# Kernel tuning notes

Hardware: AMD Instinct MI355X
Metric: run time of the kernel (lower is better)

Reference implementation:

```python
import jax, jax.numpy as jnp
import numpy as np

B_IMG, B_CAP, T_CAP, D = 64, 64, 64, 1024
H = D // 8          # CBN MLP bottleneck (k=8)
T_IMG = 36          # fixed number of image regions; cap_embed truncated to this
EPS = 1e-5          # BatchNorm eps
GAMMA = 10.0        # softmax gate temperature (norm_output=True)


def _l2norm(x, axis=-1):
    return x / jnp.linalg.norm(x, axis=axis, keepdims=True)


def setup_inputs() -> dict:
    key = jax.random.key(0)
    ks = jax.random.split(key, 8)
    s1 = 1.0 / np.sqrt(D)
    s2 = 1.0 / np.sqrt(H)
    return {
        "img_embed": jax.random.normal(ks[0], (B_IMG, T_IMG, D), jnp.float32),
        "cap_embed": jax.random.normal(ks[1], (B_CAP, T_CAP, D), jnp.float32),
        "lens": jax.random.randint(ks[2], (B_CAP,), 1, T_CAP + 1).astype(jnp.int32),
        # CondBatchNorm1d gamma/beta predictor MLPs: Linear(D,H)->ReLU->Linear(H,D)
        "Wg1": jax.random.normal(ks[3], (D, H), jnp.float32) * s1,
        "bg1": jnp.zeros((H,), jnp.float32),
        "Wg2": jax.random.normal(ks[4], (H, D), jnp.float32) * s2,
        "bg2": jnp.zeros((D,), jnp.float32),
        "Wb1": jax.random.normal(ks[5], (D, H), jnp.float32) * s1,
        "bb1": jnp.zeros((H,), jnp.float32),
        "Wb2": jax.random.normal(ks[6], (H, D), jnp.float32) * s2,
        "bb2": jnp.zeros((D,), jnp.float32),
    }


def reference(img_embed, cap_embed, lens, Wg1, bg1, Wg2, bg2, Wb1, bb1, Wb2, bb2):
    # permute to channels-first and truncate captions to 36 timesteps
    cap = jnp.transpose(cap_embed, (0, 2, 1))[:, :, :T_IMG]   # (Bc, D, 36)
    img = jnp.transpose(img_embed, (0, 2, 1))                 # (Bi, D, 36)
    img_repr = img.mean(-1)                                   # (Bi, D)

    # BatchNorm1d (affine=False), training-mode batch stats over (Bc, T) per channel.
    # cap is identical across the original per-image loop, so normalize once.
    mu = cap.mean(axis=(0, 2), keepdims=True)
    var = cap.var(axis=(0, 2), keepdims=True)
    xn = (cap - mu) / jnp.sqrt(var + EPS)                     # (Bc, D, 36)

    # condition-dependent gamma/beta per image (CBN: 1 + delta_gamma)
    gam = 1.0 + (jax.nn.relu(img_repr @ Wg1 + bg1) @ Wg2 + bg2)   # (Bi, D)
    bet = jax.nn.relu(img_repr @ Wb1 + bb1) @ Wb2 + bb2           # (Bi, D)

    # vectorized over the original Python loop: (Bi, Bc, D, 36)
    txt = gam[:, None, :, None] * xn[None] + bet[:, None, :, None]
    mask = jax.nn.softmax(txt * GAMMA, axis=-1)               # gate over time axis
    txt_vec = (mask * txt).mean(-1)                           # (Bi, Bc, D)

    txt_vec = _l2norm(txt_vec, -1)
    img_vec = _l2norm(img_repr, -1)                           # (Bi, D)
    sims = jnp.einsum("id,ibd->ib", img_vec, txt_vec)        # (Bi, Bc)
    return sims
```

## Files before the change

kernel.cpp:

```cpp
#include <hip/hip_runtime.h>
#include <hip/hip_bf16.h>

#define BI 64
#define BC 64
#define TCAP 64
#define D 1024
#define H 128
#define TIMG 36

__global__ __launch_bounds__(256) void k_pre(const float* __restrict__ img,
                                             const float* __restrict__ cap,
                                             const float* __restrict__ Wg1,
                                             const float* __restrict__ Wb1,
                                             float* __restrict__ repr,
                                             float* __restrict__ ivec,
                                             float* __restrict__ part,
                                             float* __restrict__ W1T) {
    int blk = blockIdx.x, tid = threadIdx.x;
    if (blk < 64) {
        int i = blk;
        const float4* base = (const float4*)(img + (size_t)i * TIMG * D);
        float4 s = {0.f, 0.f, 0.f, 0.f};
        for (int t = 0; t < TIMG; ++t) {
            float4 v = base[t * 256 + tid];
            s.x += v.x; s.y += v.y; s.z += v.z; s.w += v.w;
        }
        s.x *= (1.f / 36.f); s.y *= (1.f / 36.f); s.z *= (1.f / 36.f); s.w *= (1.f / 36.f);
        ((float4*)(repr + (size_t)i * D))[tid] = s;
        float local = s.x * s.x + s.y * s.y + s.z * s.z + s.w * s.w;
        for (int off = 32; off; off >>= 1) local += __shfl_xor(local, off);
        __shared__ float red[4];
        int wave = tid >> 6;
        if ((tid & 63) == 0) red[wave] = local;
        __syncthreads();
        float inv = rsqrtf(red[0] + red[1] + red[2] + red[3]);
        float4 o = {s.x * inv, s.y * inv, s.z * inv, s.w * inv};
        ((float4*)(ivec + (size_t)i * D))[tid] = o;
    } else if (blk < 128) {
        int b = blk - 64;
        const float4* base = (const float4*)(cap + (size_t)b * TCAP * D);
        float4 s = {0.f, 0.f, 0.f, 0.f}, ss = {0.f, 0.f, 0.f, 0.f};
        for (int t = 0; t < TIMG; ++t) {
            float4 v = base[t * 256 + tid];
            s.x += v.x; s.y += v.y; s.z += v.z; s.w += v.w;
            ss.x = fmaf(v.x, v.x, ss.x); ss.y = fmaf(v.y, v.y, ss.y);
            ss.z = fmaf(v.z, v.z, ss.z); ss.w = fmaf(v.w, v.w, ss.w);
        }
        ((float4*)(part + b * 2048))[tid] = s;
        ((float4*)(part + b * 2048 + 1024))[tid] = ss;
    } else {
        __shared__ float tile[64][65];
        int idx = blk - 128;
        int bx = idx & 15, by = (idx >> 4) & 1, bz = idx >> 5;
        const float* W = bz ? Wb1 : Wg1;
        int d0 = bx * 64, c0 = by * 64;
        int lane = tid & 63, w = tid >> 6;
#pragma unroll
        for (int k = 0; k < 16; ++k) {
            int dl = k * 4 + w;
            tile[dl][lane] = W[(size_t)(d0 + dl) * H + c0 + lane];
        }
        __syncthreads();
#pragma unroll
        for (int k = 0; k < 16; ++k) {
            int cl = k * 4 + w;
            W1T[(size_t)(bz * 128 + c0 + cl) * D + d0 + lane] = tile[lane][cl];
        }
    }
}

__global__ __launch_bounds__(256) void k_mid(const float* __restrict__ part,
                                             const float* __restrict__ repr,
                                             const float* __restrict__ W1T,
                                             const float* __restrict__ bg1,
                                             const float* __restrict__ bb1,
                                             float* __restrict__ mu,
                                             float* __restrict__ istd,
                                             float* __restrict__ hid) {
    int blk = blockIdx.x, tid = threadIdx.x;
    if (blk < 4) {
        int d = blk * 256 + tid;
        float s = 0.f, ss = 0.f;
        for (int g = 0; g < BC; ++g) {
            s += part[g * 2048 + d];
            ss += part[g * 2048 + 1024 + d];
        }
        const float invN = 1.f / 2304.f;
        float m = s * invN;
        float v = ss * invN - m * m;
        mu[d] = m;
        istd[d] = rsqrtf(v + 1e-5f);
    } else {
        int o = (blk - 4) * 4 + (tid >> 6);
        int lane = tid & 63;
        int i = o >> 8, c = o & 255;
        const float4* r = (const float4*)(repr + (size_t)i * D);
        const float4* w = (const float4*)(W1T + (size_t)c * D);
        float acc = 0.f;
#pragma unroll
        for (int k = 0; k < 4; ++k) {
            float4 rv = r[k * 64 + lane];
            float4 wv = w[k * 64 + lane];
            acc = fmaf(rv.x, wv.x, acc);
            acc = fmaf(rv.y, wv.y, acc);
            acc = fmaf(rv.z, wv.z, acc);
            acc = fmaf(rv.w, wv.w, acc);
        }
        for (int off = 32; off; off >>= 1) acc += __shfl_xor(acc, off);
        if (lane == 0) {
            float b = (c < 128) ? bg1[c] : bb1[c - 128];
            hid[o] = fmaxf(acc + b, 0.f);
        }
    }
}

__global__ __launch_bounds__(128) void k_out(const float* __restrict__ hid,
                                             const float* __restrict__ Wg2, const float* __restrict__ bg2,
                                             const float* __restrict__ Wb2, const float* __restrict__ bb2,
                                             float* __restrict__ gam, float* __restrict__ bet) {
    int i = blockIdx.x >> 2;
    int d2 = (blockIdx.x & 3) * 128 + threadIdx.x;
    __shared__ float h[256];
    h[threadIdx.x] = hid[i * 256 + threadIdx.x];
    h[128 + threadIdx.x] = hid[i * 256 + 128 + threadIdx.x];
    __syncthreads();
    float2 g = ((const float2*)bg2)[d2];
    float2 bb = ((const float2*)bb2)[d2];
#pragma unroll 4
    for (int hh = 0; hh < H; ++hh) {
        float2 wg = ((const float2*)(Wg2 + (size_t)hh * D))[d2];
        float2 wb = ((const float2*)(Wb2 + (size_t)hh * D))[d2];
        float hg = h[hh], hb = h[128 + hh];
        g.x = fmaf(hg, wg.x, g.x);
        g.y = fmaf(hg, wg.y, g.y);
        bb.x = fmaf(hb, wb.x, bb.x);
        bb.y = fmaf(hb, wb.y, bb.y);
    }
    float2 go = {1.f + g.x, 1.f + g.y};
    ((float2*)(gam + (size_t)i * D))[d2] = go;
    ((float2*)(bet + (size_t)i * D))[d2] = bb;
}

__global__ __launch_bounds__(512, 1) void k_main(const float* __restrict__ cap,
                                                 const float* __restrict__ mu,
                                                 const float* __restrict__ istd,
                                                 const float* __restrict__ gam,
                                                 const float* __restrict__ bet,
                                                 const float* __restrict__ ivec,
                                                 float* __restrict__ out) {
    int b = blockIdx.x, ig = blockIdx.y, tid = threadIdx.x;
    const float2* base = (const float2*)(cap + (size_t)b * TCAP * D);
    float2 mu2 = ((const float2*)mu)[tid];
    float2 is2 = ((const float2*)istd)[tid];
    const float A = 14.4269504089f;
    const float INV = 0.0693147180560f;

    float a0[16], a1[16], c0[16], c1[16];
    float sw0[16], sw1[16], sxa0[16], sxa1[16];
#pragma unroll
    for (int k = 0; k < 16; ++k) {
        int i = ig * 16 + k;
        float2 g = ((const float2*)(gam + (size_t)i * D))[tid];
        float2 be = ((const float2*)(bet + (size_t)i * D))[tid];
        a0[k] = A * g.x;
        a1[k] = A * g.y;
        c0[k] = A * (be.x - 6.f);
        c1[k] = A * (be.y - 6.f);
        sw0[k] = 0.f; sw1[k] = 0.f; sxa0[k] = 0.f; sxa1[k] = 0.f;
    }
#pragma unroll 2
    for (int t = 0; t < TIMG; ++t) {
        float2 cp = base[t * 512 + tid];
        float x0 = (cp.x - mu2.x) * is2.x;
        float x1 = (cp.y - mu2.y) * is2.y;
#pragma unroll
        for (int k = 0; k < 16; ++k) {
            float arg0 = fmaf(a0[k], x0, c0[k]);
            float e0 = __builtin_amdgcn_exp2f(arg0);
            sw0[k] += e0;
            sxa0[k] = fmaf(e0, arg0, sxa0[k]);
            float arg1 = fmaf(a1[k], x1, c1[k]);
            float e1 = __builtin_amdgcn_exp2f(arg1);
            sw1[k] += e1;
            sxa1[k] = fmaf(e1, arg1, sxa1[k]);
        }
    }
    __shared__ float redS[16][8], redD[16][8];
    int wave = tid >> 6;
#pragma unroll
    for (int k = 0; k < 16; ++k) {
        int i = ig * 16 + k;
        float2 iv = ((const float2*)(ivec + (size_t)i * D))[tid];
        float tv0 = fmaf(INV, sxa0[k] / sw0[k], 6.f);
        float tv1 = fmaf(INV, sxa1[k] / sw1[k], 6.f);
        float ss = tv0 * tv0 + tv1 * tv1;
        float sd = iv.x * tv0 + iv.y * tv1;
        for (int off = 32; off; off >>= 1) {
            ss += __shfl_xor(ss, off);
            sd += __shfl_xor(sd, off);
        }
        if ((tid & 63) == 0) { redS[k][wave] = ss; redD[k][wave] = sd; }
    }
    __syncthreads();
    if (tid < 128) {
        int k = tid >> 3, w = tid & 7;
        float s = redS[k][w], d = redD[k][w];
#pragma unroll
        for (int off = 1; off < 8; off <<= 1) {
            s += __shfl_xor(s, off);
            d += __shfl_xor(d, off);
        }
        if (w == 0) {
            int i = ig * 16 + k;
            out[i * BC + b] = d * rsqrtf(s);
        }
    }
}

extern "C" void kernel_launch(void* const* d_in, const int* in_sizes, int n_in,
                              void* d_out, int out_size, void* d_ws, size_t ws_size,
                              hipStream_t stream) {
    const float* img = (const float*)d_in[0];
    const float* cap = (const float*)d_in[1];
    const float* Wg1 = (const float*)d_in[3];
    const float* bg1 = (const float*)d_in[4];
    const float* Wg2 = (const float*)d_in[5];
    const float* bg2 = (const float*)d_in[6];
    const float* Wb1 = (const float*)d_in[7];
    const float* bb1 = (const float*)d_in[8];
    const float* Wb2 = (const float*)d_in[9];
    const float* bb2 = (const float*)d_in[10];

    float* ws = (float*)d_ws;
    float* repr = ws;
    float* ivec = ws + 65536;
    float* gam  = ws + 131072;
    float* bet  = ws + 196608;
    float* mu   = ws + 262144;
    float* istd = ws + 263168;
    float* part = ws + 264192;
    float* W1T  = ws + 395264;
    float* hid  = ws + 657408;
    float* out = (float*)d_out;

    k_pre<<<dim3(192), dim3(256), 0, stream>>>(img, cap, Wg1, Wb1, repr, ivec, part, W1T);
    k_mid<<<dim3(4100), dim3(256), 0, stream>>>(part, repr, W1T, bg1, bb1, mu, istd, hid);
    k_out<<<dim3(256), dim3(128), 0, stream>>>(hid, Wg2, bg2, Wb2, bb2, gam, bet);
    k_main<<<dim3(BC, 4), dim3(512), 0, stream>>>(cap, mu, istd, gam, bet, ivec, out);
}
```

Before: 55.96 us.

## Split pre-reductions across more blocks and drop beta from softmax inner loop

The image-mean and caption-stat reductions are split over time chunks across more blocks, and the partial sums are finalized in the middle kernel. Each hidden-layer block now rebuilds its image representation from the partials in shared memory. The main kernel uses the fact that the softmax over time is shift-invariant, so beta can be left out of the exponent and added back after normalization. This frees the per-image c registers, and launch bounds are raised to allow two blocks per CU. The cost is more partial-buffer traffic and redundant partial summing in the matvec blocks, and the exponent now has no beta offset, which changes its range.

```diff
diff --git a/kernel.cpp b/kernel.cpp
--- a/kernel.cpp
+++ b/kernel.cpp
@@ -12,21 +12,88 @@
                                              const float* __restrict__ cap,
                                              const float* __restrict__ Wg1,
                                              const float* __restrict__ Wb1,
-                                             float* __restrict__ repr,
-                                             float* __restrict__ ivec,
-                                             float* __restrict__ part,
+                                             float* __restrict__ part_img,
+                                             float* __restrict__ part_cap,
                                              float* __restrict__ W1T) {
     int blk = blockIdx.x, tid = threadIdx.x;
-    if (blk < 64) {
-        int i = blk;
-        const float4* base = (const float4*)(img + (size_t)i * TIMG * D);
+    if (blk < 256) {
+        int i = blk >> 2, tq = blk & 3;
+        const float4* base = (const float4*)(img + (size_t)i * TIMG * D) + tq * 9 * 256;
         float4 s = {0.f, 0.f, 0.f, 0.f};
-        for (int t = 0; t < TIMG; ++t) {
+#pragma unroll
+        for (int t = 0; t < 9; ++t) {
             float4 v = base[t * 256 + tid];
             s.x += v.x; s.y += v.y; s.z += v.z; s.w += v.w;
         }
         s.x *= (1.f / 36.f); s.y *= (1.f / 36.f); s.z *= (1.f / 36.f); s.w *= (1.f / 36.f);
-        ((float4*)(repr + (size_t)i * D))[tid] = s;
+        ((float4*)part_img)[(i * 4 + tq) * 256 + tid] = s;
+    } else if (blk < 384) {
+        int idx = blk - 256;
+        int b = idx >> 1, th = idx & 1;
+        const float4* base = (const float4*)(cap + (size_t)b * TCAP * D) + th * 18 * 256;
+        float4 s = {0.f, 0.f, 0.f, 0.f}, ss = {0.f, 0.f, 0.f, 0.f};
+#pragma unroll 2
+        for (int t = 0; t < 18; ++t) {
+            float4 v = base[t * 256 + tid];
+            s.x += v.x; s.y += v.y; s.z += v.z; s.w += v.w;
+            ss.x = fmaf(v.x, v.x, ss.x); ss.y = fmaf(v.y, v.y, ss.y);
+            ss.z = fmaf(v.z, v.z, ss.z); ss.w = fmaf(v.w, v.w, ss.w);
+        }
+        ((float4*)(part_cap + (size_t)idx * 2048))[tid] = s;
+        ((float4*)(part_cap + (size_t)idx * 2048 + 1024))[tid] = ss;
+    } else {
+        __shared__ float tile[64][65];
+        int idx = blk - 384;
+        int bx = idx & 15, by = (idx >> 4) & 1, bz = idx >> 5;
+        const float* W = bz ? Wb1 : Wg1;
+        int d0 = bx * 64, c0 = by * 64;
+        int lane = tid & 63, w = tid >> 6;
+#pragma unroll
+        for (int k = 0; k < 16; ++k) {
+            int dl = k * 4 + w;
+            tile[dl][lane] = W[(size_t)(d0 + dl) * H + c0 + lane];
+        }
+        __syncthreads();
+#pragma unroll
+        for (int k = 0; k < 16; ++k) {
+            int cl = k * 4 + w;
+            W1T[(size_t)(bz * 128 + c0 + cl) * D + d0 + lane] = tile[lane][cl];
+        }
+    }
+}
+
+__global__ __launch_bounds__(256) void k_mid(const float* __restrict__ part_cap,
+                                             const float* __restrict__ part_img,
+                                             const float* __restrict__ W1T,
+                                             const float* __restrict__ bg1,
+                                             const float* __restrict__ bb1,
+                                             float* __restrict__ mu,
+                                             float* __restrict__ istd,
+                                             float* __restrict__ ivec,
+                                             float* __restrict__ hid) {
+    int blk = blockIdx.x, tid = threadIdx.x;
+    if (blk < 4) {
+        int d = blk * 256 + tid;
+        float s = 0.f, ss = 0.f;
+#pragma unroll 4
+        for (int g = 0; g < 128; ++g) {
+            s += part_cap[(size_t)g * 2048 + d];
+            ss += part_cap[(size_t)g * 2048 + 1024 + d];
+        }
+        const float invN = 1.f / 2304.f;
+        float m = s * invN;
+        float v = ss * invN - m * m;
+        mu[d] = m;
+        istd[d] = rsqrtf(v + 1e-5f);
+    } else if (blk < 68) {
+        int i = blk - 4;
+        const float4* p4 = (const float4*)part_img;
+        float4 s = {0.f, 0.f, 0.f, 0.f};
+#pragma unroll
+        for (int q = 0; q < 4; ++q) {
+            float4 v = p4[(i * 4 + q) * 256 + tid];
+            s.x += v.x; s.y += v.y; s.z += v.z; s.w += v.w;
+        }
         float local = s.x * s.x + s.y * s.y + s.z * s.z + s.w * s.w;
         for (int off = 32; off; off >>= 1) local += __shfl_xor(local, off);
         __shared__ float red[4];
@@ -36,80 +103,39 @@
         float inv = rsqrtf(red[0] + red[1] + red[2] + red[3]);
         float4 o = {s.x * inv, s.y * inv, s.z * inv, s.w * inv};
         ((float4*)(ivec + (size_t)i * D))[tid] = o;
-    } else if (blk < 128) {
-        int b = blk - 64;
-        const float4* base = (const float4*)(cap + (size_t)b * TCAP * D);
-        float4 s = {0.f, 0.f, 0.f, 0.f}, ss = {0.f, 0.f, 0.f, 0.f};
-        for (int t = 0; t < TIMG; ++t) {
-            float4 v = base[t * 256 + tid];
-            s.x += v.x; s.y += v.y; s.z += v.z; s.w += v.w;
-            ss.x = fmaf(v.x, v.x, ss.x); ss.y = fmaf(v.y, v.y, ss.y);
-            ss.z = fmaf(v.z, v.z, ss.z); ss.w = fmaf(v.w, v.w, ss.w);
-        }
-        ((float4*)(part + b * 2048))[tid] = s;
-        ((float4*)(part + b * 2048 + 1024))[tid] = ss;
     } else {
-        __shared__ float tile[64][65];
-        int idx = blk - 128;
-        int bx = idx & 15, by = (idx >> 4) & 1, bz = idx >> 5;
-        const float* W = bz ? Wb1 : Wg1;
-        int d0 = bx * 64, c0 = by * 64;
-        int lane = tid & 63, w = tid >> 6;
-#pragma unroll
-        for (int k = 0; k < 16; ++k) {
-            int dl = k * 4 + w;
-            tile[dl][lane] = W[(size_t)(d0 + dl) * H + c0 + lane];
+        int hb = blk - 68;
+        int i = hb >> 6, j = hb & 63;
+        int lane = tid & 63, wave = tid >> 6;
+        __shared__ float4 rsm[256];
+        {
+            const float4* p4 = (const float4*)part_img;
+            float4 s = {0.f, 0.f, 0.f, 0.f};
+#pragma unroll
+            for (int q = 0; q < 4; ++q) {
+                float4 v = p4[(i * 4 + q) * 256 + tid];
+                s.x += v.x; s.y += v.y; s.z += v.z; s.w += v.w;
+            }
+            rsm[tid] = s;
         }
         __syncthreads();
-#pragma unroll
-        for (int k = 0; k < 16; ++k) {
-            int cl = k * 4 + w;
-            W1T[(size_t)(bz * 128 + c0 + cl) * D + d0 + lane] = tile[lane][cl];
-        }
-    }
-}
-
-__global__ __launch_bounds__(256) void k_mid(const float* __restrict__ part,
-                                             const float* __restrict__ repr,
-                                             const float* __restrict__ W1T,
-                                             const float* __restrict__ bg1,
-                                             const float* __restrict__ bb1,
-                                             float* __restrict__ mu,
-                                             float* __restrict__ istd,
-                                             float* __restrict__ hid) {
-    int blk = blockIdx.x, tid = threadIdx.x;
-    if (blk < 4) {
-        int d = blk * 256 + tid;
-        float s = 0.f, ss = 0.f;
-        for (int g = 0; g < BC; ++g) {
-            s += part[g * 2048 + d];
-            ss += part[g * 2048 + 1024 + d];
-        }
-        const float invN = 1.f / 2304.f;
-        float m = s * invN;
-        float v = ss * invN - m * m;
-        mu[d] = m;
-        istd[d] = rsqrtf(v + 1e-5f);
-    } else {
-        int o = (blk - 4) * 4 + (tid >> 6);
-        int lane = tid & 63;
-        int i = o >> 8, c = o & 255;
-        const float4* r = (const float4*)(repr + (size_t)i * D);
-        const float4* w = (const float4*)(W1T + (size_t)c * D);
+        int c = j * 4 + wave;
+        float4 rv0 = rsm[lane], rv1 = rsm[64 + lane], rv2 = rsm[128 + lane], rv3 = rsm[192 + lane];
+        const float4* w4 = (const float4*)(W1T + (size_t)c * D);
+        float4 w0 = w4[lane], w1 = w4[64 + lane], w2 = w4[128 + lane], w3 = w4[192 + lane];
         float acc = 0.f;
-#pragma unroll
-        for (int k = 0; k < 4; ++k) {
-            float4 rv = r[k * 64 + lane];
-            float4 wv = w[k * 64 + lane];
-            acc = fmaf(rv.x, wv.x, acc);
-            acc = fmaf(rv.y, wv.y, acc);
-            acc = fmaf(rv.z, wv.z, acc);
-            acc = fmaf(rv.w, wv.w, acc);
-        }
+        acc = fmaf(rv0.x, w0.x, acc); acc = fmaf(rv0.y, w0.y, acc);
+        acc = fmaf(rv0.z, w0.z, acc); acc = fmaf(rv0.w, w0.w, acc);
+        acc = fmaf(rv1.x, w1.x, acc); acc = fmaf(rv1.y, w1.y, acc);
+        acc = fmaf(rv1.z, w1.z, acc); acc = fmaf(rv1.w, w1.w, acc);
+        acc = fmaf(rv2.x, w2.x, acc); acc = fmaf(rv2.y, w2.y, acc);
+        acc = fmaf(rv2.z, w2.z, acc); acc = fmaf(rv2.w, w2.w, acc);
+        acc = fmaf(rv3.x, w3.x, acc); acc = fmaf(rv3.y, w3.y, acc);
+        acc = fmaf(rv3.z, w3.z, acc); acc = fmaf(rv3.w, w3.w, acc);
         for (int off = 32; off; off >>= 1) acc += __shfl_xor(acc, off);
         if (lane == 0) {
-            float b = (c < 128) ? bg1[c] : bb1[c - 128];
-            hid[o] = fmaxf(acc + b, 0.f);
+            float b1v = (c < 128) ? bg1[c] : bb1[c - 128];
+            hid[i * 256 + c] = fmaxf(acc + b1v, 0.f);
         }
     }
 }
@@ -141,7 +167,7 @@
     ((float2*)(bet + (size_t)i * D))[d2] = bb;
 }
 
-__global__ __launch_bounds__(512, 1) void k_main(const float* __restrict__ cap,
+__global__ __launch_bounds__(512, 2) void k_main(const float* __restrict__ cap,
                                                  const float* __restrict__ mu,
                                                  const float* __restrict__ istd,
                                                  const float* __restrict__ gam,
@@ -153,20 +179,18 @@
     float2 mu2 = ((const float2*)mu)[tid];
     float2 is2 = ((const float2*)istd)[tid];
     const float A = 14.4269504089f;
-    const float INV = 0.0693147180560f;
-
-    float a0[16], a1[16], c0[16], c1[16];
-    float sw0[16], sw1[16], sxa0[16], sxa1[16];
+    const float M6A = -86.5617024534f;
+    const float INV_A = 0.0693147180560f;
+
+    float a0[16], a1[16];
+    float sw0[16], sw1[16], swx0[16], swx1[16];
 #pragma unroll
     for (int k = 0; k < 16; ++k) {
         int i = ig * 16 + k;
         float2 g = ((const float2*)(gam + (size_t)i * D))[tid];
-        float2 be = ((const float2*)(bet + (size_t)i * D))[tid];
         a0[k] = A * g.x;
         a1[k] = A * g.y;
-        c0[k] = A * (be.x - 6.f);
-        c1[k] = A * (be.y - 6.f);
-        sw0[k] = 0.f; sw1[k] = 0.f; sxa0[k] = 0.f; sxa1[k] = 0.f;
+        sw0[k] = 0.f; sw1[k] = 0.f; swx0[k] = 0.f; swx1[k] = 0.f;
     }
 #pragma unroll 2
     for (int t = 0; t < TIMG; ++t) {
@@ -175,14 +199,14 @@
         float x1 = (cp.y - mu2.y) * is2.y;
 #pragma unroll
         for (int k = 0; k < 16; ++k) {
-            float arg0 = fmaf(a0[k], x0, c0[k]);
+            float arg0 = fmaf(a0[k], x0, M6A);
             float e0 = __builtin_amdgcn_exp2f(arg0);
             sw0[k] += e0;
-            sxa0[k] = fmaf(e0, arg0, sxa0[k]);
-            float arg1 = fmaf(a1[k], x1, c1[k]);
+            swx0[k] = fmaf(e0, x0, swx0[k]);
+            float arg1 = fmaf(a1[k], x1, M6A);
             float e1 = __builtin_amdgcn_exp2f(arg1);
             sw1[k] += e1;
-            sxa1[k] = fmaf(e1, arg1, sxa1[k]);
+            swx1[k] = fmaf(e1, x1, swx1[k]);
         }
     }
     __shared__ float redS[16][8], redD[16][8];
@@ -191,8 +215,10 @@
     for (int k = 0; k < 16; ++k) {
         int i = ig * 16 + k;
         float2 iv = ((const float2*)(ivec + (size_t)i * D))[tid];
-        float tv0 = fmaf(INV, sxa0[k] / sw0[k], 6.f);
-        float tv1 = fmaf(INV, sxa1[k] / sw1[k], 6.f);
+        float2 be = ((const float2*)(bet + (size_t)i * D))[tid];
+        float g0 = a0[k] * INV_A, g1 = a1[k] * INV_A;
+        float tv0 = fmaf(g0, swx0[k] / sw0[k], be.x);
+        float tv1 = fmaf(g1, swx1[k] / sw1[k], be.y);
         float ss = tv0 * tv0 + tv1 * tv1;
         float sd = iv.x * tv0 + iv.y * tv1;
         for (int off = 32; off; off >>= 1) {
@@ -232,19 +258,20 @@
     const float* bb2 = (const float*)d_in[10];
 
     float* ws = (float*)d_ws;
-    float* repr = ws;
-    float* ivec = ws + 65536;
-    float* gam  = ws + 131072;
-    float* bet  = ws + 196608;
-    float* mu   = ws + 262144;
-    float* istd = ws + 263168;
-    float* part = ws + 264192;
-    float* W1T  = ws + 395264;
-    float* hid  = ws + 657408;
+    float* ivec     = ws;
+    float* gam      = ws + 65536;
+    float* bet      = ws + 131072;
+    float* mu       = ws + 196608;
+    float* istd     = ws + 197632;
+    float* part_cap = ws + 198656;
+    float* part_img = ws + 460800;
+    float* W1T      = ws + 722944;
+    float* hid      = ws + 985088;
     float* out = (float*)d_out;
 
-    k_pre<<<dim3(192), dim3(256), 0, stream>>>(img, cap, Wg1, Wb1, repr, ivec, part, W1T);
-    k_mid<<<dim3(4100), dim3(256), 0, stream>>>(part, repr, W1T, bg1, bb1, mu, istd, hid);
+    k_pre<<<dim3(448), dim3(256), 0, stream>>>(img, cap, Wg1, Wb1, part_img, part_cap, W1T);
+    k_mid<<<dim3(4164), dim3(256), 0, stream>>>(part_cap, part_img, W1T, bg1, bb1,
+                                                mu, istd, ivec, hid);
     k_out<<<dim3(256), dim3(128), 0, stream>>>(hid, Wg2, bg2, Wb2, bb2, gam, bet);
     k_main<<<dim3(BC, 4), dim3(512), 0, stream>>>(cap, mu, istd, gam, bet, ivec, out);
 }
```

After: 71.21 us. 1.27x slower.
